# Performance work log

Measured on AMD Instinct MI355X. Metric: run time of the kernel, lower is better.

## Reference

```python
import jax, jax.numpy as jnp
import numpy as np
import math

B, P, L, LMAX = 8, 64, 32, 2048
IN_DIM, TE_DIM = 12, 20
POINT = IN_DIM + TE_DIM  # 32
HID = 128
TTCN = HID - 1  # 127
NHEAD = 4
NLAYER = 2
DFF = 2048  # torch TransformerEncoderLayer default dim_feedforward
NQ = 5
TAU = 300.0
DELTA = 5.0 * 60.0  # delta_minutes=5 -> seconds


def _pe_table(M, D):
    pos = np.arange(M, dtype=np.float32)[:, None]
    div = np.exp(np.arange(0, D, 2, dtype=np.float32) * (-math.log(10000.0) / D))
    pe = np.zeros((M, D), np.float32)
    pe[:, 0::2] = np.sin(pos * div)
    pe[:, 1::2] = np.cos(pos * div)
    return jnp.asarray(pe)


def _time_bias(M):
    idx = np.arange(M, dtype=np.float32)
    dist = np.abs(idx[:, None] - idx[None, :]) * DELTA
    return jnp.asarray(np.log(np.exp(-dist / TAU) + 1e-12).astype(np.float32))


def _ln(x, g, b):
    m = jnp.mean(x, axis=-1, keepdims=True)
    v = jnp.var(x, axis=-1, keepdims=True)
    return (x - m) * jax.lax.rsqrt(v + 1e-5) * g + b


def _mha(qx, kx, vx, Wq, bq, Wk, bk, Wv, bv, Wo, bo, bias=None, key_pad=None):
    Bq, Mq, D = qx.shape
    Mk = kx.shape[1]
    dh = D // NHEAD
    q = (qx @ Wq + bq).reshape(Bq, Mq, NHEAD, dh).transpose(0, 2, 1, 3)
    k = (kx @ Wk + bk).reshape(Bq, Mk, NHEAD, dh).transpose(0, 2, 1, 3)
    v = (vx @ Wv + bv).reshape(Bq, Mk, NHEAD, dh).transpose(0, 2, 1, 3)
    s = jnp.einsum('bhqd,bhkd->bhqk', q, k) / math.sqrt(dh)
    if bias is not None:
        s = s + bias[None, None]
    if key_pad is not None:
        s = jnp.where(key_pad[:, None, None, :], -1e9, s)
    a = jax.nn.softmax(s, axis=-1)
    o = jnp.einsum('bhqk,bhkd->bhqd', a, v).transpose(0, 2, 1, 3).reshape(Bq, Mq, D)
    return o @ Wo + bo


def forward_fn(data_sequence, ts_sequence, patch_mask, patch_index, num_batch,
               te_scale_W, te_scale_b, te_per_W, te_per_b,
               fg_W1, fg_b1, fg_W2, fg_b2, fg_W3, fg_b3, T_bias,
               ga_Wq, ga_bq, ga_Wk, ga_bk, ga_Wv, ga_bv, ga_Wo, ga_bo,
               tf_Wq, tf_bq, tf_Wk, tf_bk, tf_Wv, tf_bv, tf_Wo, tf_bo,
               tf_ln1_g, tf_ln1_b, tf_ff_W1, tf_ff_b1, tf_ff_W2, tf_ff_b2,
               tf_ln2_g, tf_ln2_b,
               cls_query, cls_Wq, cls_bq, cls_Wk, cls_bk, cls_Wv, cls_bv,
               cls_Wo, cls_bo, cls_out_W, cls_out_b):
    # --- patchify_by_len, vectorized: per-patch lengths -> cumsum starts + gather ---
    mvalid = patch_mask > 0
    lens = jnp.where(mvalid, jnp.maximum(patch_index, 0), 0)
    starts = jnp.cumsum(lens, axis=1) - lens  # exclusive cumsum (B,P)
    lar = jnp.arange(L)
    idx = starts[:, :, None] + lar[None, None, :]  # (B,P,L)
    valid = (lar[None, None, :] < lens[:, :, None]) & (idx < num_batch[:, None, None]) & mvalid[:, :, None]
    idx_c = jnp.clip(idx, 0, LMAX - 1).reshape(B, P * L)
    Xg = jnp.take_along_axis(data_sequence, idx_c[:, :, None], axis=1).reshape(B, P, L, IN_DIM)
    tsg = jnp.take_along_axis(ts_sequence, idx_c, axis=1).reshape(B, P, L, 1)
    mask_pt = valid.astype(jnp.float32)[..., None]  # (B,P,L,1)
    X_patch = Xg * mask_pt
    ts_patch = tsg * mask_pt
    # --- LearnableTE ---
    te = jnp.concatenate([ts_patch @ te_scale_W + te_scale_b,
                          jnp.sin(ts_patch @ te_per_W + te_per_b)], axis=-1)
    X_int = jnp.concatenate([X_patch, te], axis=-1).reshape(B * P, L, POINT)
    mask2 = mask_pt.reshape(B * P, L, 1)
    # --- TTCN: MLP-generated dynamic filters, masked softmax over timesteps ---
    h = jax.nn.relu(X_int @ fg_W1 + fg_b1)
    h = jax.nn.relu(h @ fg_W2 + fg_b2)
    Filt = h @ fg_W3 + fg_b3  # (N, L, TTCN*POINT)
    Fm = Filt * mask2 + (1.0 - mask2) * -1e8
    Fs = jax.nn.softmax(Fm, axis=1).reshape(B * P, L, TTCN, POINT)
    ttcn = jnp.einsum('nlp,nltp->nt', X_int, Fs)
    h_t = jax.nn.relu(ttcn + T_bias)
    patch_exists = (jnp.sum(mask2, axis=1) > 0).astype(jnp.float32)  # (N,1)
    x = jnp.concatenate([h_t, patch_exists], axis=-1).reshape(B, P, HID)
    # --- stacked time-biased patch attention + transformer encoder ---
    tb = _time_bias(P)
    pe = _pe_table(P, HID)
    key_pad = patch_mask <= 0
    pm = patch_mask[:, :, None]
    for l in range(NLAYER):
        x_last = x
        ga = _mha(x, x, x, ga_Wq[l], ga_bq[l], ga_Wk[l], ga_bk[l],
                  ga_Wv[l], ga_bv[l], ga_Wo[l], ga_bo[l], bias=tb, key_pad=key_pad)
        x = x + ga * pm
        x = x + pe[None]
        # post-norm TransformerEncoderLayer, tf_layer=1, dropout=0 at inference
        a = _mha(x, x, x, tf_Wq[l], tf_bq[l], tf_Wk[l], tf_bk[l],
                 tf_Wv[l], tf_bv[l], tf_Wo[l], tf_bo[l])
        x = _ln(x + a, tf_ln1_g[l], tf_ln1_b[l])
        f = jax.nn.relu(x @ tf_ff_W1[l] + tf_ff_b1[l]) @ tf_ff_W2[l] + tf_ff_b2[l]
        x = _ln(x + f, tf_ln2_g[l], tf_ln2_b[l])
        x = x_last + x
        x = x * pm
    # --- 5-query cross-attention classifier ---
    q = jnp.broadcast_to(cls_query[None], (B, NQ, HID))
    z = _mha(q, x, x, cls_Wq, cls_bq, cls_Wk, cls_bk, cls_Wv, cls_bv,
             cls_Wo, cls_bo, key_pad=key_pad)
    logits = (z @ cls_out_W + cls_out_b)[..., 0]  # (B,5)
    return logits


def setup_inputs() -> dict:
    key = jax.random.key(0)
    ks = iter(jax.random.split(key, 64))
    def nrm(shape, s=0.05):
        return (jax.random.normal(next(ks), shape) * s).astype(jnp.float32)
    inp = {}
    inp['data_sequence'] = jax.random.normal(next(ks), (B, LMAX, IN_DIM), dtype=jnp.float32)
    inp['ts_sequence'] = jax.random.uniform(next(ks), (B, LMAX), dtype=jnp.float32) * 100.0
    inp['patch_mask'] = jnp.ones((B, P), jnp.float32)
    inp['patch_index'] = jax.random.randint(next(ks), (B, P), 1, L + 1)
    inp['num_batch'] = jnp.full((B,), LMAX, jnp.int32)
    inp['te_scale_W'] = nrm((1, 1), 0.5)
    inp['te_scale_b'] = nrm((1,), 0.5)
    inp['te_per_W'] = nrm((1, TE_DIM - 1), 0.5)
    inp['te_per_b'] = nrm((TE_DIM - 1,), 0.5)
    inp['fg_W1'] = nrm((POINT, TTCN)); inp['fg_b1'] = jnp.zeros((TTCN,), jnp.float32)
    inp['fg_W2'] = nrm((TTCN, TTCN)); inp['fg_b2'] = jnp.zeros((TTCN,), jnp.float32)
    inp['fg_W3'] = nrm((TTCN, POINT * TTCN)); inp['fg_b3'] = jnp.zeros((POINT * TTCN,), jnp.float32)
    inp['T_bias'] = nrm((1, TTCN), 0.5)
    for nm in ['ga_Wq', 'ga_Wk', 'ga_Wv', 'ga_Wo', 'tf_Wq', 'tf_Wk', 'tf_Wv', 'tf_Wo']:
        inp[nm] = nrm((NLAYER, HID, HID))
    for nm in ['ga_bq', 'ga_bk', 'ga_bv', 'ga_bo', 'tf_bq', 'tf_bk', 'tf_bv', 'tf_bo', 'tf_ff_b2']:
        inp[nm] = jnp.zeros((NLAYER, HID), jnp.float32)
    inp['tf_ln1_g'] = jnp.ones((NLAYER, HID), jnp.float32)
    inp['tf_ln1_b'] = jnp.zeros((NLAYER, HID), jnp.float32)
    inp['tf_ln2_g'] = jnp.ones((NLAYER, HID), jnp.float32)
    inp['tf_ln2_b'] = jnp.zeros((NLAYER, HID), jnp.float32)
    inp['tf_ff_W1'] = nrm((NLAYER, HID, DFF))
    inp['tf_ff_b1'] = jnp.zeros((NLAYER, DFF), jnp.float32)
    inp['tf_ff_W2'] = nrm((NLAYER, DFF, HID))
    inp['cls_query'] = nrm((NQ, HID), 0.5)
    for nm in ['cls_Wq', 'cls_Wk', 'cls_Wv', 'cls_Wo']:
        inp[nm] = nrm((HID, HID))
    for nm in ['cls_bq', 'cls_bk', 'cls_bv', 'cls_bo']:
        inp[nm] = jnp.zeros((HID,), jnp.float32)
    inp['cls_out_W'] = nrm((HID, 1))
    inp['cls_out_b'] = jnp.zeros((1,), jnp.float32)
    return inp


def reference(data_sequence, ts_sequence, patch_mask, patch_index, num_batch,
              te_scale_W, te_scale_b, te_per_W, te_per_b,
              fg_W1, fg_b1, fg_W2, fg_b2, fg_W3, fg_b3, T_bias,
              ga_Wq, ga_bq, ga_Wk, ga_bk, ga_Wv, ga_bv, ga_Wo, ga_bo,
              tf_Wq, tf_bq, tf_Wk, tf_bk, tf_Wv, tf_bv, tf_Wo, tf_bo,
              tf_ln1_g, tf_ln1_b, tf_ff_W1, tf_ff_b1, tf_ff_W2, tf_ff_b2,
              tf_ln2_g, tf_ln2_b,
              cls_query, cls_Wq, cls_bq, cls_Wk, cls_bk, cls_Wv, cls_bv,
              cls_Wo, cls_bo, cls_out_W, cls_out_b):
    return forward_fn(data_sequence, ts_sequence, patch_mask, patch_index, num_batch,
                      te_scale_W, te_scale_b, te_per_W, te_per_b,
                      fg_W1, fg_b1, fg_W2, fg_b2, fg_W3, fg_b3, T_bias,
                      ga_Wq, ga_bq, ga_Wk, ga_bk, ga_Wv, ga_bv, ga_Wo, ga_bo,
                      tf_Wq, tf_bq, tf_Wk, tf_bk, tf_Wv, tf_bv, tf_Wo, tf_bo,
                      tf_ln1_g, tf_ln1_b, tf_ff_W1, tf_ff_b1, tf_ff_W2, tf_ff_b2,
                      tf_ln2_g, tf_ln2_b,
                      cls_query, cls_Wq, cls_bq, cls_Wk, cls_bk, cls_Wv, cls_bv,
                      cls_Wo, cls_bo, cls_out_W, cls_out_b)
```

## Files before the change

### kernel.cpp

```cpp
#include <hip/hip_runtime.h>
#include <math.h>

#define BB 8
#define PP 64
#define LL 32
#define LMAXX 2048
#define INDIM 12
#define PNT 32
#define HIDD 128
#define TTCNN 127
#define NPATCH 512

#define EPI_NONE 0
#define EPI_RELU 1
#define EPI_GA   2
#define EPI_ADD  3

typedef __attribute__((ext_vector_type(8))) short short8v;
typedef __attribute__((ext_vector_type(4))) float float4v;

__device__ inline unsigned short f2bf(float f) {
    unsigned int u = __float_as_uint(f);
    unsigned int r = (u + 0x7FFFu + ((u >> 16) & 1u)) >> 16;
    return (unsigned short)r;
}

__global__ void tables_kernel(float* __restrict__ tb, float* __restrict__ pe)
{
    int e = blockIdx.x*256 + threadIdx.x;
    if (e < 64*64) {
        int i = e >> 6, j = e & 63;
        float dist = fabsf((float)(i - j)) * (300.0f / 300.0f);
        tb[e] = logf(expf(-dist) + 1e-12f);
    } else if (e < 64*64 + 64*128) {
        int e2 = e - 64*64;
        int i = e2 >> 7, d = e2 & 127;
        int mm = d >> 1;
        float div = expf((float)(2*mm) * (-logf(10000.f)/128.f));
        float ang = (float)i * div;
        pe[e2] = (d & 1) ? cosf(ang) : sinf(ang);
    }
}

__global__ void w3t_kernel(const float* __restrict__ W3, unsigned short* __restrict__ W3TB)
{
    int e = blockIdx.x*256 + threadIdx.x;
    if (e >= 4096*128) return;
    int kk = e >> 12, cidx = e & 4095;
    float v = (kk < TTCNN && cidx < 4064) ? W3[kk*4064 + cidx] : 0.f;
    W3TB[cidx*128 + kk] = f2bf(v);
}

__global__ void prep_h2_kernel(const float* __restrict__ data, const float* __restrict__ ts,
                               const float* __restrict__ pmask, const int* __restrict__ pindex,
                               const int* __restrict__ nbatch,
                               const float* __restrict__ teW, const float* __restrict__ teB,
                               const float* __restrict__ tePW, const float* __restrict__ tePB,
                               const float* __restrict__ W1, const float* __restrict__ b1,
                               const float* __restrict__ W2, const float* __restrict__ b2,
                               float* __restrict__ xint, float* __restrict__ maskout,
                               unsigned short* __restrict__ h2o)
{
    int n = blockIdx.x;
    int b = n >> 6, p = n & 63;
    __shared__ int s_start, s_len;
    __shared__ float s_mk[LL];
    __shared__ alignas(16) float Xs[LL*36];
    __shared__ alignas(16) float H1[LL*128];
    int tid = threadIdx.x;
    if (tid == 0) {
        int start = 0;
        for (int j = 0; j < p; ++j) {
            float mv = pmask[b*PP + j];
            int pi = pindex[b*PP + j];
            start += (mv > 0.f) ? (pi > 0 ? pi : 0) : 0;
        }
        float mvp = pmask[b*PP + p];
        int pip = pindex[b*PP + p];
        s_len = (mvp > 0.f) ? (pip > 0 ? pip : 0) : 0;
        s_start = start;
    }
    __syncthreads();
    int start = s_start, len = s_len, nb2 = nbatch[b];
    if (tid < LL) {
        int l = tid;
        int idx = start + l;
        float v = (l < len && idx < nb2) ? 1.f : 0.f;
        s_mk[l] = v;
        maskout[n*LL + l] = v;
    }
    __syncthreads();
    for (int e = tid; e < LL*PNT; e += 128) {
        int l = e >> 5, d = e & 31;
        float mv = s_mk[l];
        int idx = start + l;
        if (idx < 0) idx = 0;
        if (idx > LMAXX-1) idx = LMAXX-1;
        float val;
        if (d < INDIM) {
            val = (mv > 0.f) ? data[(b*LMAXX + idx)*INDIM + d] : 0.f;
        } else {
            float tsm = (mv > 0.f) ? ts[b*LMAXX + idx] : 0.f;
            if (d == INDIM) val = tsm * teW[0] + teB[0];
            else { int j = d - INDIM - 1; val = sinf(tsm * tePW[j] + tePB[j]); }
        }
        Xs[l*36 + d] = val;
        xint[n*(LL*PNT) + e] = val;
    }
    __syncthreads();
    int j = tid;
    float acc[LL];
    if (j < TTCNN) {
        #pragma unroll
        for (int l = 0; l < LL; ++l) acc[l] = b1[j];
        for (int d4 = 0; d4 < 8; ++d4) {
            float w0 = W1[(d4*4+0)*TTCNN + j];
            float w1 = W1[(d4*4+1)*TTCNN + j];
            float w2 = W1[(d4*4+2)*TTCNN + j];
            float w3 = W1[(d4*4+3)*TTCNN + j];
            #pragma unroll
            for (int l = 0; l < LL; ++l) {
                float4 x = *(float4*)&Xs[l*36 + d4*4];
                acc[l] = fmaf(x.x, w0, acc[l]);
                acc[l] = fmaf(x.y, w1, acc[l]);
                acc[l] = fmaf(x.z, w2, acc[l]);
                acc[l] = fmaf(x.w, w3, acc[l]);
            }
        }
        #pragma unroll
        for (int l = 0; l < LL; ++l) H1[l*128 + j] = fmaxf(acc[l], 0.f);
    } else {
        #pragma unroll
        for (int l = 0; l < LL; ++l) H1[l*128 + 127] = 0.f;
    }
    __syncthreads();
    if (j < TTCNN) {
        #pragma unroll
        for (int l = 0; l < LL; ++l) acc[l] = b2[j];
        for (int k4 = 0; k4 < 32; ++k4) {
            int k = k4*4;
            float w0 = W2[(k+0)*TTCNN + j];
            float w1 = W2[(k+1)*TTCNN + j];
            float w2 = W2[(k+2)*TTCNN + j];
            float w3 = (k+3 < TTCNN) ? W2[(k+3)*TTCNN + j] : 0.f;
            #pragma unroll
            for (int l = 0; l < LL; ++l) {
                float4 h = *(float4*)&H1[l*128 + k];
                acc[l] = fmaf(h.x, w0, acc[l]);
                acc[l] = fmaf(h.y, w1, acc[l]);
                acc[l] = fmaf(h.z, w2, acc[l]);
                acc[l] = fmaf(h.w, w3, acc[l]);
            }
        }
        #pragma unroll
        for (int l = 0; l < LL; ++l) h2o[(n*LL + l)*128 + j] = f2bf(fmaxf(acc[l], 0.f));
    } else {
        #pragma unroll
        for (int l = 0; l < LL; ++l) h2o[(n*LL + l)*128 + 127] = 0;
    }
}

__global__ __launch_bounds__(256) void ttcn_mfma_kernel(
    const unsigned short* __restrict__ h2b,
    const float* __restrict__ xint,
    const float* __restrict__ mask,
    const unsigned short* __restrict__ w3tb,
    const float* __restrict__ b3,
    const float* __restrict__ tbias,
    float* __restrict__ x)
{
    int bid = blockIdx.x;
    int n = bid >> 3, chunk = bid & 7;
    __shared__ alignas(16) unsigned short h2s[32*136];
    __shared__ alignas(16) float Xs[32*36];
    __shared__ float mk[32];
    int tid = threadIdx.x;
    for (int f = tid; f < 512; f += 256) {
        int l = f >> 4, c16 = f & 15;
        *(short8v*)&h2s[l*136 + c16*8] = *(const short8v*)&h2b[(n*32 + l)*128 + c16*8];
    }
    {
        int l = tid >> 3, d4 = (tid & 7)*4;
        *(float4*)&Xs[l*36 + d4] = *(const float4*)&xint[n*1024 + l*32 + d4];
    }
    if (tid < 32) mk[tid] = mask[n*32 + tid];
    __syncthreads();
    if (chunk == 0 && tid == 0) {
        float e = 0.f;
        for (int l = 0; l < 32; ++l) e += mk[l];
        x[n*HIDD + 127] = (e > 0.f) ? 1.f : 0.f;
    }
    int wave = tid >> 6, lane = tid & 63;
    int li = lane & 15, hi = lane >> 4;
    short8v a[2][4];
    #pragma unroll
    for (int mt = 0; mt < 2; ++mt)
        #pragma unroll
        for (int kk = 0; kk < 4; ++kk)
            a[mt][kk] = *(short8v*)&h2s[(mt*16 + li)*136 + kk*32 + hi*8];
    float mkr[8], off8[8], xv0[8], xv1[8];
    #pragma unroll
    for (int mt = 0; mt < 2; ++mt)
        #pragma unroll
        for (int r4 = 0; r4 < 4; ++r4) {
            int i = mt*4 + r4;
            int rr = mt*16 + hi*4 + r4;
            float mv = mk[rr];
            mkr[i] = mv;
            off8[i] = (1.f - mv) * (-30.f);
            xv0[i] = Xs[rr*36 + li];
            xv1[i] = Xs[rr*36 + 16 + li];
        }
    int cwbase = chunk*512 + wave*128;
    for (int tl = 0; tl < 4; ++tl) {
        int c0 = cwbase + tl*32;
        float4v acc[2][2] = {};
        #pragma unroll
        for (int nt2 = 0; nt2 < 2; ++nt2) {
            const unsigned short* bp = &w3tb[(size_t)(c0 + nt2*16 + li)*128 + hi*8];
            #pragma unroll
            for (int kk = 0; kk < 4; ++kk) {
                short8v bf = *(const short8v*)&bp[kk*32];
                acc[0][nt2] = __builtin_amdgcn_mfma_f32_16x16x32_bf16(a[0][kk], bf, acc[0][nt2], 0, 0, 0);
                acc[1][nt2] = __builtin_amdgcn_mfma_f32_16x16x32_bf16(a[1][kk], bf, acc[1][nt2], 0, 0, 0);
            }
        }
        int t = c0 >> 5;
        float colv2 = 0.f;
        #pragma unroll
        for (int nt2 = 0; nt2 < 2; ++nt2) {
            int cglob = c0 + nt2*16 + li;
            float bv = (cglob < 4064) ? b3[cglob] : 0.f;
            float s = 0.f, w = 0.f;
            #pragma unroll
            for (int mt = 0; mt < 2; ++mt)
                #pragma unroll
                for (int r4 = 0; r4 < 4; ++r4) {
                    int i = mt*4 + r4;
                    float fm = (acc[mt][nt2][r4] + bv)*mkr[i] + off8[i];
                    float e = __expf(fm);
                    s += e;
                    w = fmaf(e, (nt2 == 0) ? xv0[i] : xv1[i], w);
                }
            s += __shfl_xor(s, 16); w += __shfl_xor(w, 16);
            s += __shfl_xor(s, 32); w += __shfl_xor(w, 32);
            colv2 = fmaf(w, __builtin_amdgcn_rcpf(s), colv2);
        }
        colv2 += __shfl_xor(colv2, 1);
        colv2 += __shfl_xor(colv2, 2);
        colv2 += __shfl_xor(colv2, 4);
        colv2 += __shfl_xor(colv2, 8);
        if (lane == 0 && t < TTCNN)
            x[n*HIDD + t] = fmaxf(colv2 + tbias[t], 0.f);
    }
}

__global__ __launch_bounds__(256) void lin32_kernel(
    const float* __restrict__ A, int lda,
    const float* __restrict__ W0, const float* __restrict__ b0,
    const float* __restrict__ W1, const float* __restrict__ b1,
    const float* __restrict__ W2, const float* __restrict__ b2,
    float* __restrict__ O0, float* __restrict__ O1, float* __restrict__ O2,
    int K, int N, int epi,
    const float* __restrict__ xres, float* __restrict__ xlast_out,
    const float* __restrict__ pmk, const float* __restrict__ pe)
{
    __shared__ alignas(16) float As[8][132];
    int tid = threadIdx.x;
    int r = tid >> 5, c = tid & 31;
    int row = blockIdx.x*8 + r;
    int col = blockIdx.z*32 + c;
    const float* W; const float* Wb; float* O;
    if (blockIdx.y == 0)      { W = W0; Wb = b0; O = O0; }
    else if (blockIdx.y == 1) { W = W1; Wb = b1; O = O1; }
    else                      { W = W2; Wb = b2; O = O2; }
    float a0 = 0.f, a1 = 0.f, a2 = 0.f, a3 = 0.f;
    for (int kc = 0; kc < K; kc += 128) {
        __syncthreads();
        {
            int lr = tid >> 5, f4 = (tid & 31)*4;
            *(float4*)&As[lr][f4] = *(const float4*)&A[(size_t)(blockIdx.x*8 + lr)*lda + kc + f4];
        }
        __syncthreads();
        const float* wp = &W[(size_t)kc*N + col];
        #pragma unroll
        for (int k4 = 0; k4 < 32; ++k4) {
            float4 av = *(float4*)&As[r][k4*4];
            float w0_ = wp[(size_t)(k4*4+0)*N];
            float w1_ = wp[(size_t)(k4*4+1)*N];
            float w2_ = wp[(size_t)(k4*4+2)*N];
            float w3_ = wp[(size_t)(k4*4+3)*N];
            a0 = fmaf(av.x, w0_, a0);
            a1 = fmaf(av.y, w1_, a1);
            a2 = fmaf(av.z, w2_, a2);
            a3 = fmaf(av.w, w3_, a3);
        }
    }
    float val = (a0 + a1) + (a2 + a3) + Wb[col];
    if (epi == EPI_NONE) {
        O[(size_t)row*N + col] = val;
    } else if (epi == EPI_RELU) {
        O[(size_t)row*N + col] = fmaxf(val, 0.f);
    } else if (epi == EPI_GA) {
        float xr = xres[row*128 + col];
        float pmv = pmk[row];
        float pev = pe[(row & 63)*128 + col];
        xlast_out[row*128 + col] = xr;
        O[row*128 + col] = xr + val*pmv + pev;
    } else {
        O[row*128 + col] = xres[row*128 + col] + val;
    }
}

__global__ void ln1_kernel(const float* __restrict__ TMP,
                           const float* __restrict__ g, const float* __restrict__ bt,
                           float* __restrict__ xout)
{
    int r = blockIdx.x, c = threadIdx.x;
    float tv = TMP[r*128 + c];
    float s = tv, s2 = tv*tv;
    for (int off = 32; off >= 1; off >>= 1) {
        s  += __shfl_xor(s,  off);
        s2 += __shfl_xor(s2, off);
    }
    __shared__ float red[2][2];
    int w = c >> 6;
    if ((c & 63) == 0) { red[w][0] = s; red[w][1] = s2; }
    __syncthreads();
    float st  = red[0][0] + red[1][0];
    float s2t = red[0][1] + red[1][1];
    float mean = st * (1.f/128.f);
    float var = s2t * (1.f/128.f) - mean*mean;
    xout[r*128 + c] = (tv - mean)*rsqrtf(var + 1e-5f)*g[c] + bt[c];
}

__global__ __launch_bounds__(256) void ff2p32_kernel(
    const float* __restrict__ A,
    const float* __restrict__ W,
    float* __restrict__ PART)
{
    __shared__ alignas(16) float As[8][260];
    int tid = threadIdx.x;
    int r = tid >> 5, c = tid & 31;
    int ct = blockIdx.z & 3, kz = blockIdx.z >> 2;
    int row = blockIdx.x*8 + r;
    int col = ct*32 + c;
    int k0 = kz*256;
    {
        int lr = tid >> 5, f4 = (tid & 31)*4;
        const float* ap = &A[(size_t)(blockIdx.x*8 + lr)*2048 + k0];
        *(float4*)&As[lr][f4]       = *(const float4*)&ap[f4];
        *(float4*)&As[lr][128 + f4] = *(const float4*)&ap[128 + f4];
    }
    __syncthreads();
    const float* wp = &W[(size_t)k0*128 + col];
    float a0 = 0.f, a1 = 0.f, a2 = 0.f, a3 = 0.f;
    #pragma unroll 16
    for (int k4 = 0; k4 < 64; ++k4) {
        float4 av = *(float4*)&As[r][k4*4];
        float w0_ = wp[(size_t)(k4*4+0)*128];
        float w1_ = wp[(size_t)(k4*4+1)*128];
        float w2_ = wp[(size_t)(k4*4+2)*128];
        float w3_ = wp[(size_t)(k4*4+3)*128];
        a0 = fmaf(av.x, w0_, a0);
        a1 = fmaf(av.y, w1_, a1);
        a2 = fmaf(av.z, w2_, a2);
        a3 = fmaf(av.w, w3_, a3);
    }
    PART[((size_t)kz*512 + row)*128 + col] = (a0 + a1) + (a2 + a3);
}

__global__ void ln2f_kernel(const float* __restrict__ PART, const float* __restrict__ b2,
                            const float* __restrict__ xres, const float* __restrict__ xlast,
                            const float* __restrict__ pmk,
                            const float* __restrict__ g, const float* __restrict__ bt,
                            float* __restrict__ xout)
{
    int r = blockIdx.x, c = threadIdx.x;
    float v = b2[c];
    #pragma unroll
    for (int z = 0; z < 8; ++z) v += PART[((size_t)z*512 + r)*128 + c];
    float tv = xres[r*128 + c] + v;
    float s = tv, s2 = tv*tv;
    for (int off = 32; off >= 1; off >>= 1) {
        s  += __shfl_xor(s,  off);
        s2 += __shfl_xor(s2, off);
    }
    __shared__ float red[2][2];
    int w = c >> 6;
    if ((c & 63) == 0) { red[w][0] = s; red[w][1] = s2; }
    __syncthreads();
    float st  = red[0][0] + red[1][0];
    float s2t = red[0][1] + red[1][1];
    float mean = st * (1.f/128.f);
    float var = s2t * (1.f/128.f) - mean*mean;
    float y = (tv - mean)*rsqrtf(var + 1e-5f)*g[c] + bt[c];
    xout[r*128 + c] = (xlast[r*128 + c] + y)*pmk[r];
}

__global__ __launch_bounds__(256) void attn_kernel(
    const float* __restrict__ q, const float* __restrict__ k, const float* __restrict__ v,
    float* __restrict__ out, const float* __restrict__ tb,
    const float* __restrict__ pmk, int flags)
{
    int bid = blockIdx.x;
    int b = bid >> 3, h = (bid >> 1) & 3, half = bid & 1;
    int rbase = half*32;
    __shared__ alignas(16) float qs[32*36];
    __shared__ alignas(16) float ks[64*36];
    __shared__ alignas(16) float vs[64*36];
    __shared__ float as_[32*68];
    int tid = threadIdx.x;
    {
        int m = tid >> 3, d4 = (tid & 7)*4;
        *(float4*)&qs[m*36 + d4] = *(const float4*)&q[(b*64 + rbase + m)*128 + h*32 + d4];
    }
    for (int f = tid; f < 512; f += 256) {
        int m = f >> 3, d4 = (f & 7)*4;
        int gofs = (b*64 + m)*128 + h*32 + d4;
        *(float4*)&ks[m*36 + d4] = *(const float4*)&k[gofs];
        *(float4*)&vs[m*36 + d4] = *(const float4*)&v[gofs];
    }
    __syncthreads();
    int r = tid >> 3, qd = tid & 7;
    float sreg[8];
    #pragma unroll
    for (int j = 0; j < 8; ++j) {
        int cc = j*8 + qd;
        float acc = 0.f;
        #pragma unroll
        for (int d4 = 0; d4 < 8; ++d4) {
            float4 a = *(float4*)&qs[r*36 + d4*4];
            float4 bb = *(float4*)&ks[cc*36 + d4*4];
            acc += a.x*bb.x + a.y*bb.y + a.z*bb.z + a.w*bb.w;
        }
        float s = acc * 0.17677669529663687f;
        if (flags & 1) s += tb[(rbase + r)*64 + cc];
        if (flags & 2) { if (pmk[b*64 + cc] <= 0.f) s = -1e9f; }
        sreg[j] = s;
    }
    float m = sreg[0];
    #pragma unroll
    for (int j = 1; j < 8; ++j) m = fmaxf(m, sreg[j]);
    m = fmaxf(m, __shfl_xor(m, 1));
    m = fmaxf(m, __shfl_xor(m, 2));
    m = fmaxf(m, __shfl_xor(m, 4));
    float ssum = 0.f;
    #pragma unroll
    for (int j = 0; j < 8; ++j) { sreg[j] = __expf(sreg[j] - m); ssum += sreg[j]; }
    ssum += __shfl_xor(ssum, 1);
    ssum += __shfl_xor(ssum, 2);
    ssum += __shfl_xor(ssum, 4);
    float inv = __builtin_amdgcn_rcpf(ssum);
    #pragma unroll
    for (int j = 0; j < 8; ++j) as_[r*68 + j*8 + qd] = sreg[j]*inv;
    __syncthreads();
    float o0 = 0.f, o1 = 0.f, o2 = 0.f, o3 = 0.f;
    int d0 = qd*4;
    for (int cc = 0; cc < 64; ++cc) {
        float a = as_[r*68 + cc];
        float4 v4 = *(float4*)&vs[cc*36 + d0];
        o0 += a*v4.x; o1 += a*v4.y; o2 += a*v4.z; o3 += a*v4.w;
    }
    *(float4*)&out[(b*64 + rbase + r)*128 + h*32 + d0] = make_float4(o0, o1, o2, o3);
}

__global__ __launch_bounds__(256) void cls_attn_kernel(
    const float* __restrict__ clsq, const float* __restrict__ Wq, const float* __restrict__ bq,
    const float* __restrict__ k, const float* __restrict__ v,
    const float* __restrict__ pmk,
    const float* __restrict__ Wo, const float* __restrict__ bo,
    const float* __restrict__ WoutW, const float* __restrict__ boutB,
    float* __restrict__ outp)
{
    int b = blockIdx.x;
    __shared__ alignas(16) float ks[64*132];
    __shared__ alignas(16) float vs[64*132];
    __shared__ alignas(16) float q5[5*132];
    __shared__ float cq[5*128];
    __shared__ float sb[5*68];
    __shared__ float z[5*132];
    __shared__ float wef[129];
    int tid = threadIdx.x;
    for (int f = tid; f < 64*32; f += 256) {
        int m = f >> 5, d4 = (f & 31)*4;
        *(float4*)&ks[m*132 + d4] = *(const float4*)&k[(b*64+m)*128 + d4];
        *(float4*)&vs[m*132 + d4] = *(const float4*)&v[(b*64+m)*128 + d4];
    }
    for (int e = tid; e < 5*128; e += 256) {
        cq[e] = clsq[e];
        z[(e >> 7)*132 + (e & 127)] = 0.f;
    }
    __syncthreads();
    for (int it = tid; it < 5*128; it += 256) {
        int qr = it >> 7, d = it & 127;
        float a = bq[d];
        for (int kk = 0; kk < 128; ++kk) a += cq[qr*128 + kk]*Wq[kk*128 + d];
        q5[qr*132 + d] = a;
    }
    if (tid < 128) {
        float s = 0.f;
        for (int cc = 0; cc < 128; ++cc) s += Wo[tid*128 + cc]*WoutW[cc];
        wef[tid] = s;
    } else if (tid == 128) {
        float t = boutB[0];
        for (int cc = 0; cc < 128; ++cc) t += bo[cc]*WoutW[cc];
        wef[128] = t;
    }
    __syncthreads();
    for (int h = 0; h < 4; ++h) {
        for (int it = tid; it < 5*64; it += 256) {
            int qr = it >> 6, cc = it & 63;
            float acc = 0.f;
            #pragma unroll
            for (int d4 = 0; d4 < 8; ++d4) {
                float4 a = *(float4*)&q5[qr*132 + h*32 + d4*4];
                float4 bb = *(float4*)&ks[cc*132 + h*32 + d4*4];
                acc += a.x*bb.x + a.y*bb.y + a.z*bb.z + a.w*bb.w;
            }
            float s = acc * 0.17677669529663687f;
            if (pmk[b*64 + cc] <= 0.f) s = -1e9f;
            sb[qr*68 + cc] = s;
        }
        __syncthreads();
        if (tid < 5) {
            float m = -3e38f;
            for (int cc = 0; cc < 64; ++cc) m = fmaxf(m, sb[tid*68 + cc]);
            float ssum = 0.f;
            for (int cc = 0; cc < 64; ++cc) {
                float e = __expf(sb[tid*68 + cc] - m);
                sb[tid*68 + cc] = e;
                ssum += e;
            }
            float inv = __builtin_amdgcn_rcpf(ssum);
            for (int cc = 0; cc < 64; ++cc) sb[tid*68 + cc] *= inv;
        }
        __syncthreads();
        for (int it = tid; it < 5*32; it += 256) {
            int qr = it >> 5, d = it & 31;
            float acc = 0.f;
            for (int cc = 0; cc < 64; ++cc) acc += sb[qr*68 + cc]*vs[cc*132 + h*32 + d];
            z[qr*132 + h*32 + d] = acc;
        }
        __syncthreads();
    }
    if (tid < 5) {
        float acc = wef[128];
        for (int d = 0; d < 128; ++d) acc += z[tid*132 + d]*wef[d];
        outp[b*5 + tid] = acc;
    }
}

extern "C" void kernel_launch(void* const* d_in, const int* in_sizes, int n_in,
                              void* d_out, int out_size, void* d_ws, size_t ws_size,
                              hipStream_t stream)
{
    (void)n_in; (void)out_size; (void)ws_size;
    #define FP(i) ((const float*)d_in[i])
    const float* data = FP(0);
    const float* ts   = FP(1);
    const float* pmask= FP(2);
    const int*   pidx = (const int*)d_in[3];
    const int*   nb   = (const int*)d_in[4];
    const float* teW  = FP(5);
    const float* teB  = FP(6);
    const float* tePW = FP(7);
    const float* tePB = FP(8);
    const float* fgW1 = FP(9);
    const float* fgb1 = FP(10);
    const float* fgW2 = FP(11);
    const float* fgb2 = FP(12);
    const float* fgW3 = FP(13);
    const float* fgb3 = FP(14);
    const float* Tb   = FP(15);
    const float *gaWq,*gaWk,*gaWv,*gaWo,*tfWq,*tfWk,*tfWv,*tfWo;
    const float *gabq,*gabk,*gabv,*gabo,*tfbq,*tfbk,*tfbv,*tfbo,*ffb2;
    const float *ln1g,*ln1b,*ln2g,*ln2b,*ffW1,*ffb1,*ffW2;
    const float *clsq,*clsWq,*clsWk,*clsWv,*clsWo,*clsbq,*clsbk,*clsbv,*clsbo,*cloW,*clob;
    if (in_sizes[17] == 2*128*128) {
        gaWq=FP(16); gaWk=FP(17); gaWv=FP(18); gaWo=FP(19);
        tfWq=FP(20); tfWk=FP(21); tfWv=FP(22); tfWo=FP(23);
        gabq=FP(24); gabk=FP(25); gabv=FP(26); gabo=FP(27);
        tfbq=FP(28); tfbk=FP(29); tfbv=FP(30); tfbo=FP(31);
        ffb2=FP(32); ln1g=FP(33); ln1b=FP(34); ln2g=FP(35); ln2b=FP(36);
        ffW1=FP(37); ffb1=FP(38); ffW2=FP(39);
        clsq=FP(40); clsWq=FP(41); clsWk=FP(42); clsWv=FP(43); clsWo=FP(44);
        clsbq=FP(45); clsbk=FP(46); clsbv=FP(47); clsbo=FP(48); cloW=FP(49); clob=FP(50);
    } else {
        gaWq=FP(16); gabq=FP(17); gaWk=FP(18); gabk=FP(19);
        gaWv=FP(20); gabv=FP(21); gaWo=FP(22); gabo=FP(23);
        tfWq=FP(24); tfbq=FP(25); tfWk=FP(26); tfbk=FP(27);
        tfWv=FP(28); tfbv=FP(29); tfWo=FP(30); tfbo=FP(31);
        ln1g=FP(32); ln1b=FP(33); ffW1=FP(34); ffb1=FP(35); ffW2=FP(36); ffb2=FP(37);
        ln2g=FP(38); ln2b=FP(39);
        clsq=FP(40); clsWq=FP(41); clsbq=FP(42); clsWk=FP(43); clsbk=FP(44);
        clsWv=FP(45); clsbv=FP(46); clsWo=FP(47); clsbo=FP(48); cloW=FP(49); clob=FP(50);
    }

    float* ws   = (float*)d_ws;
    float* XINT = ws;
    float* PART = ws;
    float* MASK = ws + 524288;
    unsigned short* W3TB = (unsigned short*)(ws + 540672);
    unsigned short* H2Bb = (unsigned short*)(ws + 1060864);
    float* X    = ws + 3158016;
    float* XLAST= X + 65536;
    float* Q    = XLAST + 65536;
    float* Kb   = Q + 65536;
    float* Vb   = Kb + 65536;
    float* ATT  = Vb + 65536;
    float* HIDB = ATT + 65536;
    float* TBT  = HIDB + 1048576;
    float* PET  = TBT + 4096;

    tables_kernel<<<48, 256, 0, stream>>>(TBT, PET);
    w3t_kernel<<<2048, 256, 0, stream>>>(fgW3, W3TB);
    prep_h2_kernel<<<512, 128, 0, stream>>>(data, ts, pmask, pidx, nb, teW, teB, tePW, tePB,
                                            fgW1, fgb1, fgW2, fgb2, XINT, MASK, H2Bb);
    ttcn_mfma_kernel<<<4096, 256, 0, stream>>>(H2Bb, XINT, MASK, W3TB, fgb3, Tb, X);

    for (int l = 0; l < 2; ++l) {
        const float* Wq = gaWq + l*16384; const float* bq = gabq + l*128;
        const float* Wk = gaWk + l*16384; const float* bk = gabk + l*128;
        const float* Wv = gaWv + l*16384; const float* bv = gabv + l*128;
        const float* Wo = gaWo + l*16384; const float* bo = gabo + l*128;
        lin32_kernel<<<dim3(64,3,4), 256, 0, stream>>>(X, 128, Wq,bq, Wk,bk, Wv,bv, Q,Kb,Vb,
            128,128, EPI_NONE, nullptr,nullptr,nullptr,nullptr);
        attn_kernel<<<64, 256, 0, stream>>>(Q, Kb, Vb, ATT, TBT, pmask, 3);
        lin32_kernel<<<dim3(64,1,4), 256, 0, stream>>>(ATT, 128, Wo,bo, Wo,bo, Wo,bo, X,X,X,
            128,128, EPI_GA, X, XLAST, pmask, PET);
        const float* Wq2 = tfWq + l*16384; const float* bq2 = tfbq + l*128;
        const float* Wk2 = tfWk + l*16384; const float* bk2 = tfbk + l*128;
        const float* Wv2 = tfWv + l*16384; const float* bv2 = tfbv + l*128;
        const float* Wo2 = tfWo + l*16384; const float* bo2 = tfbo + l*128;
        lin32_kernel<<<dim3(64,3,4), 256, 0, stream>>>(X, 128, Wq2,bq2, Wk2,bk2, Wv2,bv2, Q,Kb,Vb,
            128,128, EPI_NONE, nullptr,nullptr,nullptr,nullptr);
        attn_kernel<<<64, 256, 0, stream>>>(Q, Kb, Vb, ATT, TBT, pmask, 0);
        lin32_kernel<<<dim3(64,1,4), 256, 0, stream>>>(ATT, 128, Wo2,bo2, Wo2,bo2, Wo2,bo2, Q,Q,Q,
            128,128, EPI_ADD, X, nullptr, nullptr, nullptr);
        ln1_kernel<<<512, 128, 0, stream>>>(Q, ln1g + l*128, ln1b + l*128, X);
        lin32_kernel<<<dim3(64,1,64), 256, 0, stream>>>(X, 128,
            ffW1 + (size_t)l*128*2048, ffb1 + l*2048, ffW1, ffb1, ffW1, ffb1, HIDB,HIDB,HIDB,
            128,2048, EPI_RELU, nullptr,nullptr,nullptr,nullptr);
        ff2p32_kernel<<<dim3(64,1,32), 256, 0, stream>>>(HIDB, ffW2 + (size_t)l*2048*128, PART);
        ln2f_kernel<<<512, 128, 0, stream>>>(PART, ffb2 + l*128, X, XLAST, pmask,
                                             ln2g + l*128, ln2b + l*128, X);
    }

    lin32_kernel<<<dim3(64,2,4), 256, 0, stream>>>(X, 128, clsWk,clsbk, clsWv,clsbv, clsWv,clsbv,
        Kb,Vb,Vb, 128,128, EPI_NONE, nullptr,nullptr,nullptr,nullptr);
    cls_attn_kernel<<<8, 256, 0, stream>>>(clsq, clsWq, clsbq, Kb, Vb, pmask,
                                           clsWo, clsbo, cloW, clob, (float*)d_out);
}
```

Baseline: 467.7 us.

## Fuse transformer layer stages into per-row mega kernels

Merges the table and W3-transpose setup kernels into one launch. Fuses the graph-attention output projection, residual, positional add and the next QKV projection into one kernel. Fuses the transformer output projection, LN1, FFN1+ReLU, FFN2, LN2 and the next layer's (or classifier's) K/V projection into a single 4-row-per-block kernel with the hidden activations kept in shared memory. This removes many launches and the global round-trip of the 2048-wide hidden buffer and split-K partials, but runs the FFN with only 128 blocks, each streaming the full FFN weights, which reduces parallelism.

```diff
diff --git a/kernel.cpp b/kernel.cpp
--- a/kernel.cpp
+++ b/kernel.cpp
@@ -25,30 +25,30 @@
     return (unsigned short)r;
 }
 
-__global__ void tables_kernel(float* __restrict__ tb, float* __restrict__ pe)
-{
-    int e = blockIdx.x*256 + threadIdx.x;
-    if (e < 64*64) {
-        int i = e >> 6, j = e & 63;
-        float dist = fabsf((float)(i - j)) * (300.0f / 300.0f);
-        tb[e] = logf(expf(-dist) + 1e-12f);
-    } else if (e < 64*64 + 64*128) {
-        int e2 = e - 64*64;
-        int i = e2 >> 7, d = e2 & 127;
-        int mm = d >> 1;
-        float div = expf((float)(2*mm) * (-logf(10000.f)/128.f));
-        float ang = (float)i * div;
-        pe[e2] = (d & 1) ? cosf(ang) : sinf(ang);
-    }
-}
-
-__global__ void w3t_kernel(const float* __restrict__ W3, unsigned short* __restrict__ W3TB)
-{
-    int e = blockIdx.x*256 + threadIdx.x;
-    if (e >= 4096*128) return;
-    int kk = e >> 12, cidx = e & 4095;
-    float v = (kk < TTCNN && cidx < 4064) ? W3[kk*4064 + cidx] : 0.f;
-    W3TB[cidx*128 + kk] = f2bf(v);
+__global__ void tables_w3t_kernel(const float* __restrict__ W3, unsigned short* __restrict__ W3TB,
+                                  float* __restrict__ tb, float* __restrict__ pe)
+{
+    int bid = blockIdx.x;
+    if (bid < 2048) {
+        int e = bid*256 + threadIdx.x;
+        int kk = e >> 12, cidx = e & 4095;
+        float v = (kk < TTCNN && cidx < 4064) ? W3[kk*4064 + cidx] : 0.f;
+        W3TB[cidx*128 + kk] = f2bf(v);
+    } else {
+        int e = (bid - 2048)*256 + threadIdx.x;
+        if (e < 64*64) {
+            int i = e >> 6, j = e & 63;
+            float dist = fabsf((float)(i - j));
+            tb[e] = logf(expf(-dist) + 1e-12f);
+        } else if (e < 64*64 + 64*128) {
+            int e2 = e - 64*64;
+            int i = e2 >> 7, d = e2 & 127;
+            int mm = d >> 1;
+            float div = expf((float)(2*mm) * (-logf(10000.f)/128.f));
+            float ang = (float)i * div;
+            pe[e2] = (d & 1) ? cosf(ang) : sinf(ang);
+        }
+    }
 }
 
 __global__ void prep_h2_kernel(const float* __restrict__ data, const float* __restrict__ ts,
@@ -312,90 +312,235 @@
     }
 }
 
-__global__ void ln1_kernel(const float* __restrict__ TMP,
-                           const float* __restrict__ g, const float* __restrict__ bt,
-                           float* __restrict__ xout)
-{
-    int r = blockIdx.x, c = threadIdx.x;
-    float tv = TMP[r*128 + c];
-    float s = tv, s2 = tv*tv;
-    for (int off = 32; off >= 1; off >>= 1) {
-        s  += __shfl_xor(s,  off);
-        s2 += __shfl_xor(s2, off);
-    }
-    __shared__ float red[2][2];
-    int w = c >> 6;
-    if ((c & 63) == 0) { red[w][0] = s; red[w][1] = s2; }
-    __syncthreads();
-    float st  = red[0][0] + red[1][0];
-    float s2t = red[0][1] + red[1][1];
-    float mean = st * (1.f/128.f);
-    float var = s2t * (1.f/128.f) - mean*mean;
-    xout[r*128 + c] = (tv - mean)*rsqrtf(var + 1e-5f)*g[c] + bt[c];
-}
-
-__global__ __launch_bounds__(256) void ff2p32_kernel(
-    const float* __restrict__ A,
-    const float* __restrict__ W,
-    float* __restrict__ PART)
-{
-    __shared__ alignas(16) float As[8][260];
+__global__ __launch_bounds__(256) void gaqkv_kernel(
+    const float* __restrict__ ATT, const float* __restrict__ X,
+    const float* __restrict__ pmk, const float* __restrict__ pe,
+    const float* __restrict__ Wo, const float* __restrict__ bo,
+    const float* __restrict__ Wq, const float* __restrict__ bq,
+    const float* __restrict__ Wk, const float* __restrict__ bk,
+    const float* __restrict__ Wv, const float* __restrict__ bv,
+    float* __restrict__ Xout, float* __restrict__ XLASTo,
+    float* __restrict__ Qo, float* __restrict__ Ko, float* __restrict__ Vo)
+{
+    __shared__ alignas(16) float att4[4][132];
+    __shared__ alignas(16) float xf[4][132];
     int tid = threadIdx.x;
-    int r = tid >> 5, c = tid & 31;
-    int ct = blockIdx.z & 3, kz = blockIdx.z >> 2;
-    int row = blockIdx.x*8 + r;
-    int col = ct*32 + c;
-    int k0 = kz*256;
-    {
+    int r0 = blockIdx.x*4;
+    if (tid < 128) {
         int lr = tid >> 5, f4 = (tid & 31)*4;
-        const float* ap = &A[(size_t)(blockIdx.x*8 + lr)*2048 + k0];
-        *(float4*)&As[lr][f4]       = *(const float4*)&ap[f4];
-        *(float4*)&As[lr][128 + f4] = *(const float4*)&ap[128 + f4];
-    }
-    __syncthreads();
-    const float* wp = &W[(size_t)k0*128 + col];
-    float a0 = 0.f, a1 = 0.f, a2 = 0.f, a3 = 0.f;
-    #pragma unroll 16
-    for (int k4 = 0; k4 < 64; ++k4) {
-        float4 av = *(float4*)&As[r][k4*4];
-        float w0_ = wp[(size_t)(k4*4+0)*128];
-        float w1_ = wp[(size_t)(k4*4+1)*128];
-        float w2_ = wp[(size_t)(k4*4+2)*128];
-        float w3_ = wp[(size_t)(k4*4+3)*128];
-        a0 = fmaf(av.x, w0_, a0);
-        a1 = fmaf(av.y, w1_, a1);
-        a2 = fmaf(av.z, w2_, a2);
-        a3 = fmaf(av.w, w3_, a3);
-    }
-    PART[((size_t)kz*512 + row)*128 + col] = (a0 + a1) + (a2 + a3);
-}
-
-__global__ void ln2f_kernel(const float* __restrict__ PART, const float* __restrict__ b2,
-                            const float* __restrict__ xres, const float* __restrict__ xlast,
-                            const float* __restrict__ pmk,
-                            const float* __restrict__ g, const float* __restrict__ bt,
-                            float* __restrict__ xout)
-{
-    int r = blockIdx.x, c = threadIdx.x;
-    float v = b2[c];
-    #pragma unroll
-    for (int z = 0; z < 8; ++z) v += PART[((size_t)z*512 + r)*128 + c];
-    float tv = xres[r*128 + c] + v;
-    float s = tv, s2 = tv*tv;
-    for (int off = 32; off >= 1; off >>= 1) {
-        s  += __shfl_xor(s,  off);
-        s2 += __shfl_xor(s2, off);
-    }
-    __shared__ float red[2][2];
-    int w = c >> 6;
-    if ((c & 63) == 0) { red[w][0] = s; red[w][1] = s2; }
-    __syncthreads();
-    float st  = red[0][0] + red[1][0];
-    float s2t = red[0][1] + red[1][1];
-    float mean = st * (1.f/128.f);
-    float var = s2t * (1.f/128.f) - mean*mean;
-    float y = (tv - mean)*rsqrtf(var + 1e-5f)*g[c] + bt[c];
-    xout[r*128 + c] = (xlast[r*128 + c] + y)*pmk[r];
+        *(float4*)&att4[lr][f4] = *(const float4*)&ATT[(r0 + lr)*128 + f4];
+    } else {
+        int t = tid - 128;
+        int lr = t >> 5, f4 = (t & 31)*4;
+        *(float4*)&xf[lr][f4] = *(const float4*)&X[(r0 + lr)*128 + f4];
+    }
+    __syncthreads();
+    int col = tid & 127, rp = tid >> 7;
+    float a0 = bo[col], a1 = bo[col];
+    #pragma unroll 8
+    for (int k = 0; k < 128; ++k) {
+        float w = Wo[k*128 + col];
+        a0 = fmaf(att4[rp][k], w, a0);
+        a1 = fmaf(att4[rp+2][k], w, a1);
+    }
+    int gr0 = r0 + rp, gr1 = r0 + rp + 2;
+    float x0 = xf[rp][col], x1 = xf[rp+2][col];
+    XLASTo[gr0*128 + col] = x0;
+    XLASTo[gr1*128 + col] = x1;
+    float xn0 = x0 + a0*pmk[gr0] + pe[(gr0 & 63)*128 + col];
+    float xn1 = x1 + a1*pmk[gr1] + pe[(gr1 & 63)*128 + col];
+    Xout[gr0*128 + col] = xn0;
+    Xout[gr1*128 + col] = xn1;
+    xf[rp][col] = xn0;
+    xf[rp+2][col] = xn1;
+    __syncthreads();
+    float q0 = bq[col], q1 = bq[col];
+    float k0 = bk[col], k1 = bk[col];
+    float v0 = bv[col], v1 = bv[col];
+    #pragma unroll 4
+    for (int k = 0; k < 128; ++k) {
+        float xa = xf[rp][k], xb = xf[rp+2][k];
+        float wq = Wq[k*128 + col];
+        float wk = Wk[k*128 + col];
+        float wv = Wv[k*128 + col];
+        q0 = fmaf(xa, wq, q0); q1 = fmaf(xb, wq, q1);
+        k0 = fmaf(xa, wk, k0); k1 = fmaf(xb, wk, k1);
+        v0 = fmaf(xa, wv, v0); v1 = fmaf(xb, wv, v1);
+    }
+    Qo[gr0*128 + col] = q0; Qo[gr1*128 + col] = q1;
+    Ko[gr0*128 + col] = k0; Ko[gr1*128 + col] = k1;
+    Vo[gr0*128 + col] = v0; Vo[gr1*128 + col] = v1;
+}
+
+__global__ __launch_bounds__(256) void megaff_kernel(
+    const float* __restrict__ ATT, const float* __restrict__ X,
+    const float* __restrict__ XLAST, const float* __restrict__ pmk,
+    const float* __restrict__ Wo, const float* __restrict__ bo,
+    const float* __restrict__ g1, const float* __restrict__ bt1,
+    const float* __restrict__ W1, const float* __restrict__ b1,
+    const float* __restrict__ W2, const float* __restrict__ b2,
+    const float* __restrict__ g2, const float* __restrict__ bt2,
+    const float* __restrict__ nWq, const float* __restrict__ nbq,
+    const float* __restrict__ nWk, const float* __restrict__ nbk,
+    const float* __restrict__ nWv, const float* __restrict__ nbv,
+    float* __restrict__ Xout,
+    float* __restrict__ Qo, float* __restrict__ Ko, float* __restrict__ Vo)
+{
+    __shared__ alignas(16) float att4[4][132];
+    __shared__ alignas(16) float xn[4][132];
+    __shared__ alignas(16) float tvb[4][132];
+    __shared__ alignas(16) float xfb[4][132];
+    __shared__ alignas(16) float h[4][2052];
+    int tid = threadIdx.x;
+    int r0 = blockIdx.x*4;
+    if (tid < 128) {
+        int lr = tid >> 5, f4 = (tid & 31)*4;
+        *(float4*)&att4[lr][f4] = *(const float4*)&ATT[(r0 + lr)*128 + f4];
+    } else {
+        int t = tid - 128;
+        int lr = t >> 5, f4 = (t & 31)*4;
+        *(float4*)&xn[lr][f4] = *(const float4*)&X[(r0 + lr)*128 + f4];
+    }
+    __syncthreads();
+    int col = tid & 127, rp = tid >> 7;
+    {
+        float a0 = bo[col], a1 = bo[col];
+        #pragma unroll 8
+        for (int k = 0; k < 128; ++k) {
+            float w = Wo[k*128 + col];
+            a0 = fmaf(att4[rp][k], w, a0);
+            a1 = fmaf(att4[rp+2][k], w, a1);
+        }
+        xn[rp][col]   += a0;
+        xn[rp+2][col] += a1;
+    }
+    __syncthreads();
+    {
+        int row = tid >> 6, l = tid & 63;
+        float v0 = xn[row][l], v1 = xn[row][l + 64];
+        float s = v0 + v1, s2 = v0*v0 + v1*v1;
+        for (int off = 32; off >= 1; off >>= 1) {
+            s  += __shfl_xor(s,  off);
+            s2 += __shfl_xor(s2, off);
+        }
+        float mean = s * (1.f/128.f);
+        float var = s2 * (1.f/128.f) - mean*mean;
+        float rs = rsqrtf(var + 1e-5f);
+        xn[row][l]      = (v0 - mean)*rs*g1[l] + bt1[l];
+        xn[row][l + 64] = (v1 - mean)*rs*g1[l + 64] + bt1[l + 64];
+    }
+    __syncthreads();
+    {
+        int c8 = tid*8;
+        float acc[4][8];
+        #pragma unroll
+        for (int j = 0; j < 8; ++j) {
+            float bj = b1[c8 + j];
+            #pragma unroll
+            for (int r = 0; r < 4; ++r) acc[r][j] = bj;
+        }
+        #pragma unroll 4
+        for (int k = 0; k < 128; ++k) {
+            float4 wA = *(const float4*)&W1[(size_t)k*2048 + c8];
+            float4 wB = *(const float4*)&W1[(size_t)k*2048 + c8 + 4];
+            float xk0 = xn[0][k], xk1 = xn[1][k], xk2 = xn[2][k], xk3 = xn[3][k];
+            acc[0][0] = fmaf(xk0, wA.x, acc[0][0]); acc[0][1] = fmaf(xk0, wA.y, acc[0][1]);
+            acc[0][2] = fmaf(xk0, wA.z, acc[0][2]); acc[0][3] = fmaf(xk0, wA.w, acc[0][3]);
+            acc[0][4] = fmaf(xk0, wB.x, acc[0][4]); acc[0][5] = fmaf(xk0, wB.y, acc[0][5]);
+            acc[0][6] = fmaf(xk0, wB.z, acc[0][6]); acc[0][7] = fmaf(xk0, wB.w, acc[0][7]);
+            acc[1][0] = fmaf(xk1, wA.x, acc[1][0]); acc[1][1] = fmaf(xk1, wA.y, acc[1][1]);
+            acc[1][2] = fmaf(xk1, wA.z, acc[1][2]); acc[1][3] = fmaf(xk1, wA.w, acc[1][3]);
+            acc[1][4] = fmaf(xk1, wB.x, acc[1][4]); acc[1][5] = fmaf(xk1, wB.y, acc[1][5]);
+            acc[1][6] = fmaf(xk1, wB.z, acc[1][6]); acc[1][7] = fmaf(xk1, wB.w, acc[1][7]);
+            acc[2][0] = fmaf(xk2, wA.x, acc[2][0]); acc[2][1] = fmaf(xk2, wA.y, acc[2][1]);
+            acc[2][2] = fmaf(xk2, wA.z, acc[2][2]); acc[2][3] = fmaf(xk2, wA.w, acc[2][3]);
+            acc[2][4] = fmaf(xk2, wB.x, acc[2][4]); acc[2][5] = fmaf(xk2, wB.y, acc[2][5]);
+            acc[2][6] = fmaf(xk2, wB.z, acc[2][6]); acc[2][7] = fmaf(xk2, wB.w, acc[2][7]);
+            acc[3][0] = fmaf(xk3, wA.x, acc[3][0]); acc[3][1] = fmaf(xk3, wA.y, acc[3][1]);
+            acc[3][2] = fmaf(xk3, wA.z, acc[3][2]); acc[3][3] = fmaf(xk3, wA.w, acc[3][3]);
+            acc[3][4] = fmaf(xk3, wB.x, acc[3][4]); acc[3][5] = fmaf(xk3, wB.y, acc[3][5]);
+            acc[3][6] = fmaf(xk3, wB.z, acc[3][6]); acc[3][7] = fmaf(xk3, wB.w, acc[3][7]);
+        }
+        #pragma unroll
+        for (int r = 0; r < 4; ++r) {
+            float4 o0 = make_float4(fmaxf(acc[r][0],0.f), fmaxf(acc[r][1],0.f),
+                                    fmaxf(acc[r][2],0.f), fmaxf(acc[r][3],0.f));
+            float4 o1 = make_float4(fmaxf(acc[r][4],0.f), fmaxf(acc[r][5],0.f),
+                                    fmaxf(acc[r][6],0.f), fmaxf(acc[r][7],0.f));
+            *(float4*)&h[r][c8]     = o0;
+            *(float4*)&h[r][c8 + 4] = o1;
+        }
+    }
+    __syncthreads();
+    {
+        float f0 = b2[col], f1 = b2[col];
+        #pragma unroll 8
+        for (int k = 0; k < 2048; ++k) {
+            float w = W2[(size_t)k*128 + col];
+            f0 = fmaf(h[rp][k], w, f0);
+            f1 = fmaf(h[rp+2][k], w, f1);
+        }
+        tvb[rp][col]   = xn[rp][col] + f0;
+        tvb[rp+2][col] = xn[rp+2][col] + f1;
+    }
+    __syncthreads();
+    {
+        int row = tid >> 6, l = tid & 63;
+        float v0 = tvb[row][l], v1 = tvb[row][l + 64];
+        float s = v0 + v1, s2 = v0*v0 + v1*v1;
+        for (int off = 32; off >= 1; off >>= 1) {
+            s  += __shfl_xor(s,  off);
+            s2 += __shfl_xor(s2, off);
+        }
+        float mean = s * (1.f/128.f);
+        float var = s2 * (1.f/128.f) - mean*mean;
+        float rs = rsqrtf(var + 1e-5f);
+        float y0 = (v0 - mean)*rs*g2[l] + bt2[l];
+        float y1 = (v1 - mean)*rs*g2[l + 64] + bt2[l + 64];
+        int gr = r0 + row;
+        float pmv = pmk[gr];
+        float xf0 = (XLAST[gr*128 + l]      + y0)*pmv;
+        float xf1 = (XLAST[gr*128 + l + 64] + y1)*pmv;
+        Xout[gr*128 + l]      = xf0;
+        Xout[gr*128 + l + 64] = xf1;
+        xfb[row][l]      = xf0;
+        xfb[row][l + 64] = xf1;
+    }
+    __syncthreads();
+    int gr0 = r0 + rp, gr1 = r0 + rp + 2;
+    if (nWq) {
+        float q0 = nbq[col], q1 = nbq[col];
+        #pragma unroll 8
+        for (int k = 0; k < 128; ++k) {
+            float w = nWq[k*128 + col];
+            q0 = fmaf(xfb[rp][k], w, q0);
+            q1 = fmaf(xfb[rp+2][k], w, q1);
+        }
+        Qo[gr0*128 + col] = q0;
+        Qo[gr1*128 + col] = q1;
+    }
+    {
+        float k0 = nbk[col], k1 = nbk[col];
+        #pragma unroll 8
+        for (int k = 0; k < 128; ++k) {
+            float w = nWk[k*128 + col];
+            k0 = fmaf(xfb[rp][k], w, k0);
+            k1 = fmaf(xfb[rp+2][k], w, k1);
+        }
+        Ko[gr0*128 + col] = k0;
+        Ko[gr1*128 + col] = k1;
+    }
+    {
+        float v0 = nbv[col], v1 = nbv[col];
+        #pragma unroll 8
+        for (int k = 0; k < 128; ++k) {
+            float w = nWv[k*128 + col];
+            v0 = fmaf(xfb[rp][k], w, v0);
+            v1 = fmaf(xfb[rp+2][k], w, v1);
+        }
+        Vo[gr0*128 + col] = v0;
+        Vo[gr1*128 + col] = v1;
+    }
 }
 
 __global__ __launch_bounds__(256) void attn_kernel(
@@ -599,7 +744,6 @@
 
     float* ws   = (float*)d_ws;
     float* XINT = ws;
-    float* PART = ws;
     float* MASK = ws + 524288;
     unsigned short* W3TB = (unsigned short*)(ws + 540672);
     unsigned short* H2Bb = (unsigned short*)(ws + 1060864);
@@ -609,46 +753,44 @@
     float* Kb   = Q + 65536;
     float* Vb   = Kb + 65536;
     float* ATT  = Vb + 65536;
-    float* HIDB = ATT + 65536;
-    float* TBT  = HIDB + 1048576;
+    float* TBT  = ATT + 65536;
     float* PET  = TBT + 4096;
 
-    tables_kernel<<<48, 256, 0, stream>>>(TBT, PET);
-    w3t_kernel<<<2048, 256, 0, stream>>>(fgW3, W3TB);
+    tables_w3t_kernel<<<2096, 256, 0, stream>>>(fgW3, W3TB, TBT, PET);
     prep_h2_kernel<<<512, 128, 0, stream>>>(data, ts, pmask, pidx, nb, teW, teB, tePW, tePB,
                                             fgW1, fgb1, fgW2, fgb2, XINT, MASK, H2Bb);
     ttcn_mfma_kernel<<<4096, 256, 0, stream>>>(H2Bb, XINT, MASK, W3TB, fgb3, Tb, X);
 
+    lin32_kernel<<<dim3(64,3,4), 256, 0, stream>>>(X, 128, gaWq,gabq, gaWk,gabk, gaWv,gabv, Q,Kb,Vb,
+        128,128, EPI_NONE, nullptr,nullptr,nullptr,nullptr);
+
     for (int l = 0; l < 2; ++l) {
-        const float* Wq = gaWq + l*16384; const float* bq = gabq + l*128;
-        const float* Wk = gaWk + l*16384; const float* bk = gabk + l*128;
-        const float* Wv = gaWv + l*16384; const float* bv = gabv + l*128;
-        const float* Wo = gaWo + l*16384; const float* bo = gabo + l*128;
-        lin32_kernel<<<dim3(64,3,4), 256, 0, stream>>>(X, 128, Wq,bq, Wk,bk, Wv,bv, Q,Kb,Vb,
-            128,128, EPI_NONE, nullptr,nullptr,nullptr,nullptr);
-        attn_kernel<<<64, 256, 0, stream>>>(Q, Kb, Vb, ATT, TBT, pmask, 3);
-        lin32_kernel<<<dim3(64,1,4), 256, 0, stream>>>(ATT, 128, Wo,bo, Wo,bo, Wo,bo, X,X,X,
-            128,128, EPI_GA, X, XLAST, pmask, PET);
+        const float* Wo  = gaWo + l*16384; const float* bo  = gabo + l*128;
         const float* Wq2 = tfWq + l*16384; const float* bq2 = tfbq + l*128;
         const float* Wk2 = tfWk + l*16384; const float* bk2 = tfbk + l*128;
         const float* Wv2 = tfWv + l*16384; const float* bv2 = tfbv + l*128;
         const float* Wo2 = tfWo + l*16384; const float* bo2 = tfbo + l*128;
-        lin32_kernel<<<dim3(64,3,4), 256, 0, stream>>>(X, 128, Wq2,bq2, Wk2,bk2, Wv2,bv2, Q,Kb,Vb,
-            128,128, EPI_NONE, nullptr,nullptr,nullptr,nullptr);
+        attn_kernel<<<64, 256, 0, stream>>>(Q, Kb, Vb, ATT, TBT, pmask, 3);
+        gaqkv_kernel<<<128, 256, 0, stream>>>(ATT, X, pmask, PET, Wo, bo,
+                                              Wq2, bq2, Wk2, bk2, Wv2, bv2,
+                                              X, XLAST, Q, Kb, Vb);
         attn_kernel<<<64, 256, 0, stream>>>(Q, Kb, Vb, ATT, TBT, pmask, 0);
-        lin32_kernel<<<dim3(64,1,4), 256, 0, stream>>>(ATT, 128, Wo2,bo2, Wo2,bo2, Wo2,bo2, Q,Q,Q,
-            128,128, EPI_ADD, X, nullptr, nullptr, nullptr);
-        ln1_kernel<<<512, 128, 0, stream>>>(Q, ln1g + l*128, ln1b + l*128, X);
-        lin32_kernel<<<dim3(64,1,64), 256, 0, stream>>>(X, 128,
-            ffW1 + (size_t)l*128*2048, ffb1 + l*2048, ffW1, ffb1, ffW1, ffb1, HIDB,HIDB,HIDB,
-            128,2048, EPI_RELU, nullptr,nullptr,nullptr,nullptr);
-        ff2p32_kernel<<<dim3(64,1,32), 256, 0, stream>>>(HIDB, ffW2 + (size_t)l*2048*128, PART);
-        ln2f_kernel<<<512, 128, 0, stream>>>(PART, ffb2 + l*128, X, XLAST, pmask,
-                                             ln2g + l*128, ln2b + l*128, X);
-    }
-
-    lin32_kernel<<<dim3(64,2,4), 256, 0, stream>>>(X, 128, clsWk,clsbk, clsWv,clsbv, clsWv,clsbv,
-        Kb,Vb,Vb, 128,128, EPI_NONE, nullptr,nullptr,nullptr,nullptr);
+        if (l == 0) {
+            megaff_kernel<<<128, 256, 0, stream>>>(ATT, X, XLAST, pmask,
+                Wo2, bo2, ln1g, ln1b,
+                ffW1, ffb1, ffW2, ffb2, ln2g, ln2b,
+                gaWq + 16384, gabq + 128, gaWk + 16384, gabk + 128, gaWv + 16384, gabv + 128,
+                X, Q, Kb, Vb);
+        } else {
+            megaff_kernel<<<128, 256, 0, stream>>>(ATT, X, XLAST, pmask,
+                Wo2, bo2, ln1g + 128, ln1b + 128,
+                ffW1 + (size_t)128*2048, ffb1 + 2048, ffW2 + (size_t)2048*128, ffb2 + 128,
+                ln2g + 128, ln2b + 128,
+                nullptr, nullptr, clsWk, clsbk, clsWv, clsbv,
+                X, Q, Kb, Vb);
+        }
+    }
+
     cls_attn_kernel<<<8, 256, 0, stream>>>(clsq, clsWq, clsbq, Kb, Vb, pmask,
                                            clsWo, clsbo, cloW, clob, (float*)d_out);
 }
```

Measured after the change: 577.2 us. 1.23x slower.
